# Kernel optimization log

Measured on AMD Instinct MI355X. Metric: run time of the kernel, lower is better.

The kernel has to match this reference:

```python
import jax, jax.numpy as jnp
import numpy as np

N_HEAD = 16
N_KV_HEAD = 4
N_EMBD = 2048
HEAD_DIM = N_EMBD // N_HEAD
RMS_EPS = float(np.finfo(np.float32).eps)  # torch F.rms_norm default eps


def setup_inputs() -> dict:
    key = jax.random.key(0)
    ks = jax.random.split(key, 7)
    B, T = 2, 2048
    s = 0.02
    return {
        "x": jax.random.normal(ks[0], (B, T, N_EMBD), jnp.float32),
        "cos": jax.random.uniform(ks[1], (T, 1, HEAD_DIM), jnp.float32),
        "sin": jax.random.uniform(ks[2], (T, 1, HEAD_DIM), jnp.float32),
        "wq": jax.random.normal(ks[3], (N_HEAD * HEAD_DIM, N_EMBD), jnp.float32) * s,
        "wk": jax.random.normal(ks[4], (N_KV_HEAD * HEAD_DIM, N_EMBD), jnp.float32) * s,
        "wv": jax.random.normal(ks[5], (N_KV_HEAD * HEAD_DIM, N_EMBD), jnp.float32) * s,
        "wproj": jax.random.normal(ks[6], (N_EMBD, N_EMBD), jnp.float32) * s,
    }


def _rotate_half(x):
    h = x.shape[-1] // 2
    return jnp.concatenate([-x[..., h:], x[..., :h]], axis=-1)


def _apply_rope(x, cos, sin):  # x: [B, T, H, D]; cos/sin: [T, 1, D]
    return x * cos + _rotate_half(x) * sin


def _rms_norm(x):
    var = jnp.mean(jnp.square(x), axis=-1, keepdims=True)
    return x * jax.lax.rsqrt(var + RMS_EPS)


def reference(x, cos, sin, wq, wk, wv, wproj):
    B, T, C = x.shape
    group = N_HEAD // N_KV_HEAD
    q = (x @ wq.T).reshape(B, T, N_HEAD, HEAD_DIM)
    k = (x @ wk.T).reshape(B, T, N_KV_HEAD, HEAD_DIM)
    v = (x @ wv.T).reshape(B, T, N_KV_HEAD, HEAD_DIM)
    q = _rms_norm(_apply_rope(q, cos, sin))  # RoPE then QK RMSNorm
    k = _rms_norm(_apply_rope(k, cos, sin))
    # to [B, H, T, D]; expand kv heads for GQA
    q = q.transpose(0, 2, 1, 3)
    k = jnp.repeat(k.transpose(0, 2, 1, 3), group, axis=1)
    v = jnp.repeat(v.transpose(0, 2, 1, 3), group, axis=1)
    scale = 1.0 / jnp.sqrt(jnp.asarray(HEAD_DIM, x.dtype))
    scores = jnp.einsum('bhqd,bhkd->bhqk', q, k) * scale
    causal = jnp.tril(jnp.ones((T, T), bool))
    scores = jnp.where(causal, scores, jnp.asarray(-jnp.inf, scores.dtype))
    attn = jax.nn.softmax(scores, axis=-1)
    y = jnp.einsum('bhqk,bhkd->bhqd', attn, v)
    y = y.transpose(0, 2, 1, 3).reshape(B, T, C)
    return y @ wproj.T
```

## Files before the change

### kernel.cpp

```cpp
#include <hip/hip_runtime.h>
#include <hip/hip_bf16.h>

typedef __hip_bfloat16 bf16;
typedef __attribute__((ext_vector_type(8))) __bf16 bf16x8;
typedef __attribute__((ext_vector_type(4))) float f32x4;

#define MFMA16(a, b, c) __builtin_amdgcn_mfma_f32_16x16x32_bf16((a), (b), (c), 0, 0, 0)

#define BT 4096
#define CE 2048
#define NQKV 3072
#define TSEQ 2048
#define HD 128

#define QSCALE (0.08838834764831845f * 1.4426950408889634f)
#define M2 16.3222f

__device__ __forceinline__ void gld16(const void* g, void* l)
{
    __builtin_amdgcn_global_load_lds(
        (const __attribute__((address_space(1))) void*)g,
        (__attribute__((address_space(3))) void*)l, 16, 0, 0);
}

__global__ void detect_dtype(const unsigned short* __restrict__ x, int* __restrict__ flag)
{
    __shared__ int cnt;
    if (threadIdx.x == 0) cnt = 0;
    __syncthreads();
    unsigned short w = x[2 * threadIdx.x];
    int e = (w >> 7) & 0xFF;
    atomicAdd(&cnt, (e >= 117 && e <= 130) ? 1 : 0);
    __syncthreads();
    if (threadIdx.x == 0) *flag = (cnt < 128) ? 1 : 0;
}

__device__ __forceinline__ void stage8(short* dst, const void* src, size_t eoff, bool f32)
{
    if (f32) {
        const float* s = (const float*)src + eoff;
        float4 f0 = *(const float4*)s;
        float4 f1 = *(const float4*)(s + 4);
        bf16x8 v;
        v[0] = (__bf16)f0.x; v[1] = (__bf16)f0.y; v[2] = (__bf16)f0.z; v[3] = (__bf16)f0.w;
        v[4] = (__bf16)f1.x; v[5] = (__bf16)f1.y; v[6] = (__bf16)f1.z; v[7] = (__bf16)f1.w;
        *(bf16x8*)dst = v;
    } else {
        *(uint4*)dst = *(const uint4*)((const bf16*)src + eoff);
    }
}

__device__ __forceinline__ float ldf(const void* p, int i, bool f32)
{
    return f32 ? ((const float*)p)[i] : __bfloat162float(((const bf16*)p)[i]);
}

__global__ __launch_bounds__(256)
void conv_bf16(const void* __restrict__ src, bf16* __restrict__ dst,
               const int* __restrict__ flagp)
{
    const bool f = *flagp != 0;
    size_t i8 = (size_t)blockIdx.x * 256 + threadIdx.x;
    stage8((short*)(dst + i8 * 8), src, i8 * 8, f);
}

__global__ __launch_bounds__(256)
void gemm_bt(const void* __restrict__ A, const bf16* __restrict__ W,
             void* __restrict__ C, int M, int N, int K, int lda,
             int aGate, int oGate, const int* __restrict__ flagp)
{
    __shared__ short As[128][32];
    __shared__ short Bs[128][32];

    const int f = *flagp;
    const bool aF = aGate && f, oF = oGate && f;

    const int tid   = threadIdx.x;
    const int lane  = tid & 63;
    const int wid   = tid >> 6;
    const int row16 = lane & 15;
    const int quad  = lane >> 4;
    const int wr    = wid >> 1;
    const int wc    = wid & 1;
    const int m0    = blockIdx.y * 128;
    const int n0    = blockIdx.x * 128;

    const int rl4 = wid * 16 + (lane >> 2);
    const int c8  = (lane & 3) * 8;

    f32x4 acc[4][4];
#pragma unroll
    for (int i = 0; i < 4; i++)
#pragma unroll
        for (int j = 0; j < 4; j++)
            acc[i][j] = (f32x4){0.f, 0.f, 0.f, 0.f};

    for (int k0 = 0; k0 < K; k0 += 32) {
#pragma unroll
        for (int i = 0; i < 2; i++) {
            int r = i * 64 + rl4;
            gld16(W + (size_t)(n0 + r) * K + k0 + c8, &Bs[r][c8]);
        }
        if (!aF) {
#pragma unroll
            for (int i = 0; i < 2; i++) {
                int r = i * 64 + rl4;
                gld16((const bf16*)A + (size_t)(m0 + r) * lda + k0 + c8, &As[r][c8]);
            }
        } else {
#pragma unroll
            for (int i = 0; i < 2; i++) {
                int c = i * 256 + tid;
                int row = c >> 2, col = (c & 3) << 3;
                stage8(&As[row][col], A, (size_t)(m0 + row) * lda + k0 + col, true);
            }
        }
        __syncthreads();

        bf16x8 af[4], bfv[4];
#pragma unroll
        for (int mi = 0; mi < 4; mi++)
            af[mi] = *(const bf16x8*)&As[wr * 64 + mi * 16 + row16][quad * 8];
#pragma unroll
        for (int ni = 0; ni < 4; ni++)
            bfv[ni] = *(const bf16x8*)&Bs[wc * 64 + ni * 16 + row16][quad * 8];
#pragma unroll
        for (int mi = 0; mi < 4; mi++)
#pragma unroll
            for (int ni = 0; ni < 4; ni++)
                acc[mi][ni] = MFMA16(af[mi], bfv[ni], acc[mi][ni]);
        __syncthreads();
    }

#pragma unroll
    for (int mi = 0; mi < 4; mi++) {
        int rowb = m0 + wr * 64 + mi * 16 + quad * 4;
#pragma unroll
        for (int ni = 0; ni < 4; ni++) {
            int col = n0 + wc * 64 + ni * 16 + row16;
#pragma unroll
            for (int r = 0; r < 4; r++) {
                size_t idx = (size_t)(rowb + r) * N + col;
                float  v   = acc[mi][ni][r];
                if (oF) ((float*)C)[idx] = v;
                else    ((bf16*)C)[idx]  = __float2bfloat16(v);
            }
        }
    }
}

__global__ __launch_bounds__(256, 2)
void gemm9(const bf16* __restrict__ A, const bf16* __restrict__ W,
           void* __restrict__ C, int M, int N, int K, int lda,
           int oGate, const int* __restrict__ flagp)
{
    __shared__ __bf16 As[3][128][32];
    __shared__ __bf16 Bs[3][256][32];

    const bool oF = oGate && (*flagp != 0);

    const int tid   = threadIdx.x;
    const int lane  = tid & 63;
    const int row16 = lane & 15;
    const int quad  = lane >> 4;
    const int wc    = tid >> 6;
    const int m0    = blockIdx.y * 128;
    const int n0    = blockIdx.x * 256;
    const int NT    = K >> 5;

    const int srow = tid >> 2;
    const int sc   = (tid & 3) ^ (srow & 3);
    const bf16* Ag = A + (size_t)(m0 + srow) * lda + sc * 8;
    const bf16* Bg = W + (size_t)(n0 + srow) * K   + sc * 8;
    char* const AsB = (char*)As;
    char* const BsB = (char*)Bs;
    const int sdst = tid * 16;

    auto stA = [&](int kt, int s) {
#pragma unroll
        for (int u = 0; u < 2; ++u)
            gld16(Ag + (size_t)(u * 64) * lda + kt * 32,
                  AsB + s * 8192 + u * 4096 + sdst);
    };
    auto stB = [&](int kt, int s) {
#pragma unroll
        for (int u = 0; u < 4; ++u)
            gld16(Bg + (size_t)(u * 64) * K + kt * 32,
                  BsB + s * 16384 + u * 4096 + sdst);
    };

    const int swzB  = (quad ^ (row16 & 3)) * 16;
    const int raOff = row16 * 64 + swzB;
    const int rbOff = (wc * 64 + row16) * 64 + swzB;

    f32x4 acc[8][4];
#pragma unroll
    for (int i = 0; i < 8; i++)
#pragma unroll
        for (int j = 0; j < 4; j++)
            acc[i][j] = (f32x4){0.f, 0.f, 0.f, 0.f};

    stA(0, 0); stB(0, 0);
    stA(1, 1); stB(1, 1);
    asm volatile("s_waitcnt vmcnt(6)" ::: "memory");
    __builtin_amdgcn_s_barrier();
    __builtin_amdgcn_sched_barrier(0);

    int sl = 0, sl2 = 2;
    for (int t = 0; t < NT; ++t) {
        const bool pf = (t + 2) < NT;
        const int sbA = sl * 8192, sbB = sl * 16384;

        bf16x8 af0[4], bfr[4];
#pragma unroll
        for (int ni = 0; ni < 4; ni++)
            bfr[ni] = *(const bf16x8*)(BsB + sbB + rbOff + ni * 1024);
#pragma unroll
        for (int mi = 0; mi < 4; mi++)
            af0[mi] = *(const bf16x8*)(AsB + sbA + raOff + mi * 1024);
        if (pf) stB(t + 2, sl2);
        __builtin_amdgcn_s_barrier();
        asm volatile("s_waitcnt lgkmcnt(0)" ::: "memory");
        __builtin_amdgcn_s_setprio(1);
#pragma unroll
        for (int mi = 0; mi < 4; mi++)
#pragma unroll
            for (int ni = 0; ni < 4; ni++)
                acc[mi][ni] = MFMA16(af0[mi], bfr[ni], acc[mi][ni]);
        __builtin_amdgcn_s_setprio(0);
        __builtin_amdgcn_s_barrier();
        __builtin_amdgcn_sched_barrier(0);

        bf16x8 af1[4];
#pragma unroll
        for (int mi = 0; mi < 4; mi++)
            af1[mi] = *(const bf16x8*)(AsB + sbA + raOff + (4 + mi) * 1024);
        if (pf) stA(t + 2, sl2);
        if (t < NT - 2) asm volatile("s_waitcnt vmcnt(6)" ::: "memory");
        else            asm volatile("s_waitcnt vmcnt(0)" ::: "memory");
        __builtin_amdgcn_s_barrier();
        asm volatile("s_waitcnt lgkmcnt(0)" ::: "memory");
        __builtin_amdgcn_s_setprio(1);
#pragma unroll
        for (int mi = 0; mi < 4; mi++)
#pragma unroll
            for (int ni = 0; ni < 4; ni++)
                acc[4 + mi][ni] = MFMA16(af1[mi], bfr[ni], acc[4 + mi][ni]);
        __builtin_amdgcn_s_setprio(0);
        __builtin_amdgcn_s_barrier();
        __builtin_amdgcn_sched_barrier(0);

        sl  = (sl  == 2) ? 0 : sl  + 1;
        sl2 = (sl2 == 2) ? 0 : sl2 + 1;
    }

#pragma unroll
    for (int mi = 0; mi < 8; mi++) {
        int rowb = m0 + mi * 16 + quad * 4;
#pragma unroll
        for (int ni = 0; ni < 4; ni++) {
            int col = n0 + wc * 64 + ni * 16 + row16;
#pragma unroll
            for (int r = 0; r < 4; r++) {
                size_t idx = (size_t)(rowb + r) * N + col;
                float  v   = acc[mi][ni][r];
                if (oF) ((float*)C)[idx] = v;
                else    ((bf16*)C)[idx]  = __float2bfloat16(v);
            }
        }
    }
}

__global__ __launch_bounds__(256)
void rope_rms(bf16* __restrict__ qkv, const void* __restrict__ cosp,
              const void* __restrict__ sinp, const int* __restrict__ flagp)
{
    const bool f = *flagp != 0;
    const int wg   = blockIdx.x * 4 + (threadIdx.x >> 6);
    const int lane = threadIdx.x & 63;
    const int s    = wg % 20;
    const int m    = wg / 20;
    const int t    = m & (TSEQ - 1);

    const int col = (s < 16) ? s * HD : CE + (s - 16) * HD;
    bf16* p = qkv + (size_t)m * NQKV + col;

    float xlo = __bfloat162float(p[lane]);
    float xhi = __bfloat162float(p[lane + 64]);
    float cl  = ldf(cosp, t * HD + lane, f);
    float sl  = ldf(sinp, t * HD + lane, f);
    float ch  = ldf(cosp, t * HD + 64 + lane, f);
    float sh  = ldf(sinp, t * HD + 64 + lane, f);

    float rlo = xlo * cl - xhi * sl;
    float rhi = xhi * ch + xlo * sh;

    float ss = rlo * rlo + rhi * rhi;
#pragma unroll
    for (int off = 32; off > 0; off >>= 1)
        ss += __shfl_xor(ss, off, 64);
    float inv = rsqrtf(ss * (1.0f / 128.0f) + 1.1920929e-07f);
    if (s < 16) inv *= QSCALE;

    p[lane]      = __float2bfloat16(rlo * inv);
    p[lane + 64] = __float2bfloat16(rhi * inv);
}

__global__ __launch_bounds__(256)
void vtrans(const bf16* __restrict__ qkv, bf16* __restrict__ vt)
{
    int idx = blockIdx.x * 256 + threadIdx.x;
    int t  = idx & (TSEQ - 1);
    int d  = (idx >> 11) & 127;
    int bh = idx >> 18;
    vt[idx] = qkv[((size_t)((bh >> 2) * TSEQ + t)) * NQKV + 2560 + (bh & 3) * HD + d];
}

__global__ __launch_bounds__(512, 2)
void attn(bf16* __restrict__ qkv, const bf16* __restrict__ vt)
{
    __shared__ __bf16 Ks[2][64][128];
    __shared__ __bf16 Vs[2][128][64];
    __shared__ __bf16 Pl[8][16][72];

    const int tid   = threadIdx.x;
    const int lane  = tid & 63;
    const int wid   = tid >> 6;
    const int row16 = lane & 15;
    const int quad  = lane >> 4;
    const int b   = blockIdx.y >> 2;
    const int hk  = blockIdx.y & 3;
    const int h   = hk * 4 + (wid & 3);
    const int mh  = wid >> 2;
    const int p   = blockIdx.x;

    const bf16* Kp = qkv + ((size_t)(b * TSEQ)) * NQKV + CE + hk * HD;
    const bf16* Vp = vt + ((size_t)(b * 4 + hk) * HD) * TSEQ;

    char* const KsB = (char*)Ks;
    char* const VsB = (char*)Vs;

    auto stage = [&](int buf, int k0) {
#pragma unroll
        for (int i = 0; i < 2; i++) {
            int kr = (wid << 3) + i * 4 + (lane >> 4);
            int kc = (lane & 15) ^ (kr & 7);
            gld16(Kp + (size_t)(k0 + kr) * NQKV + kc * 8,
                  KsB + buf * 16384 + ((wid << 3) + i * 4) * 256 + lane * 16);
            int vr = (wid << 4) + i * 8 + (lane >> 3);
            int vc = (lane & 7) ^ (vr & 7);
            gld16(Vp + (size_t)vr * TSEQ + k0 + vc * 8,
                  VsB + buf * 16384 + ((wid << 4) + i * 8) * 128 + lane * 16);
        }
    };

    for (int pass = 0; pass < 2; ++pass) {
        const int xi  = pass ? 63 - p : p;
        const int nkt = (xi >> 1) + 1;
        const int qr0 = xi * 32 + mh * 16;

        const bf16* Q = qkv + ((size_t)(b * TSEQ + qr0)) * NQKV + h * HD;
        bf16x8 aq[4];
#pragma unroll
        for (int ds = 0; ds < 4; ds++)
            aq[ds] = *(const bf16x8*)(Q + (size_t)row16 * NQKV + ds * 32 + quad * 8);

        f32x4 o[8];
#pragma unroll
        for (int dt = 0; dt < 8; dt++) o[dt] = (f32x4){0.f, 0.f, 0.f, 0.f};
        float lsum[4] = {0.f, 0.f, 0.f, 0.f};

        __syncthreads();
        stage(0, 0);
        __syncthreads();

        for (int t = 0; t < nkt; ++t) {
            const int cur = t & 1;
            if (t + 1 < nkt) stage(cur ^ 1, (t + 1) * 64);

            f32x4 s[4];
#pragma unroll
            for (int kg = 0; kg < 4; kg++) s[kg] = (f32x4){0.f, 0.f, 0.f, 0.f};
            __builtin_amdgcn_s_setprio(1);
#pragma unroll
            for (int ds = 0; ds < 4; ds++) {
#pragma unroll
                for (int kg = 0; kg < 4; kg++) {
                    int krow = kg * 16 + row16;
                    int phys = (ds * 4 + quad) ^ (row16 & 7);
                    bf16x8 kf = *(const bf16x8*)(KsB + cur * 16384 + krow * 256 + phys * 16);
                    s[kg] = MFMA16(aq[ds], kf, s[kg]);
                }
            }
            __builtin_amdgcn_s_setprio(0);

            const bool diag = (t == nkt - 1);
            const int  k0   = t * 64;
#pragma unroll
            for (int r = 0; r < 4; r++) {
                float pv[4];
                int qrow = qr0 + quad * 4 + r;
#pragma unroll
                for (int kg = 0; kg < 4; kg++) {
                    float e = __builtin_amdgcn_exp2f(s[kg][r] - M2);
                    pv[kg] = (!diag || (k0 + kg * 16 + row16 <= qrow)) ? e : 0.f;
                }
                lsum[r] += (pv[0] + pv[1]) + (pv[2] + pv[3]);
#pragma unroll
                for (int kg = 0; kg < 4; kg++)
                    Pl[wid][quad * 4 + r][kg * 16 + row16] = (__bf16)pv[kg];
            }
            __asm__ volatile("" ::: "memory");

            __builtin_amdgcn_s_setprio(1);
#pragma unroll
            for (int c = 0; c < 2; c++) {
                bf16x8 pf = *(const bf16x8*)&Pl[wid][row16][c * 32 + quad * 8];
#pragma unroll
                for (int dt = 0; dt < 8; dt++) {
                    int vrow = dt * 16 + row16;
                    int phys = (c * 4 + quad) ^ (row16 & 7);
                    bf16x8 vf = *(const bf16x8*)(VsB + cur * 16384 + vrow * 128 + phys * 16);
                    o[dt] = MFMA16(pf, vf, o[dt]);
                }
            }
            __builtin_amdgcn_s_setprio(0);
            __asm__ volatile("" ::: "memory");
            __syncthreads();
        }

#pragma unroll
        for (int r = 0; r < 4; r++) {
            float l = lsum[r];
#pragma unroll
            for (int off = 1; off < 16; off <<= 1)
                l += __shfl_xor(l, off, 64);
            float rl = 1.0f / l;
            int trow = qr0 + quad * 4 + r;
            bf16* dst = qkv + ((size_t)(b * TSEQ + trow)) * NQKV + h * HD;
#pragma unroll
            for (int dt = 0; dt < 8; dt++)
                dst[dt * 16 + row16] = __float2bfloat16(o[dt][r] * rl);
        }
    }
}

extern "C" void kernel_launch(void* const* d_in, const int* in_sizes, int n_in,
                              void* d_out, int out_size, void* d_ws, size_t ws_size,
                              hipStream_t stream)
{
    bf16* qkv   = (bf16*)d_ws;
    bf16* vt    = qkv + (size_t)BT * NQKV;
    bf16* wqkvb = vt + (size_t)2 * 4 * HD * TSEQ;
    int* flagp  = (int*)(wqkvb + (size_t)NQKV * CE);
    bf16* xb    = wqkvb + (size_t)NQKV * CE + 16;

    const size_t need = ((size_t)BT * NQKV + (size_t)2 * 4 * HD * TSEQ
                         + (size_t)NQKV * CE + 16 + (size_t)BT * CE) * sizeof(bf16);
    const bool useXb = ws_size >= need;

    detect_dtype<<<1, 256, 0, stream>>>((const unsigned short*)d_in[0], flagp);

    conv_bf16<<<(2048 * 2048 / 8) / 256, 256, 0, stream>>>(d_in[3], wqkvb, flagp);
    conv_bf16<<<(512 * 2048 / 8) / 256, 256, 0, stream>>>(d_in[4], wqkvb + (size_t)2048 * 2048, flagp);
    conv_bf16<<<(512 * 2048 / 8) / 256, 256, 0, stream>>>(d_in[5], wqkvb + (size_t)2560 * 2048, flagp);

    if (useXb) {
        conv_bf16<<<(BT * CE / 8) / 256, 256, 0, stream>>>(d_in[0], xb, flagp);
        gemm9<<<dim3(NQKV / 256, BT / 128), 256, 0, stream>>>(
            xb, wqkvb, qkv, BT, NQKV, CE, CE, 0, flagp);
    } else {
        gemm_bt<<<dim3(NQKV / 128, BT / 128), 256, 0, stream>>>(
            d_in[0], wqkvb, qkv, BT, NQKV, CE, CE, 1, 0, flagp);
    }

    conv_bf16<<<(2048 * 2048 / 8) / 256, 256, 0, stream>>>(d_in[6], wqkvb, flagp);

    vtrans<<<(2 * 4 * HD * TSEQ) / 256, 256, 0, stream>>>(qkv, vt);

    rope_rms<<<(BT * 20) / 4, 256, 0, stream>>>(qkv, d_in[1], d_in[2], flagp);

    attn<<<dim3(32, 2 * 4), 512, 0, stream>>>(qkv, vt);

    if (useXb) {
        gemm9<<<dim3(CE / 256, BT / 128), 256, 0, stream>>>(
            qkv, wqkvb, d_out, BT, CE, CE, NQKV, 1, flagp);
    } else {
        gemm_bt<<<dim3(CE / 128, BT / 128), 256, 0, stream>>>(
            qkv, wqkvb, d_out, BT, CE, CE, NQKV, 0, 1, flagp);
    }
}
```

Baseline: 340.0 us.

## Replace gemm9 with templated 512-thread GEMM using K=64 tiles and double buffering

Replaces the 256-thread, 3-stage, K=32 GEMM with a templated 512-thread kernel that uses K=64 LDS tiles and double buffering, with a 2x4 wave layout. The QKV projection uses 256-row tiles (MI=8) and the output projection uses 128-row tiles (MI=4). The aim is to raise MFMA work per barrier and cut synchronisation and issue overhead. In exchange, pipeline depth drops to two stages with a full vmcnt(0) wait every iteration, LDS use rises, and the larger QKV tiles mean fewer blocks in flight.

```diff
diff --git a/kernel.cpp b/kernel.cpp
--- a/kernel.cpp
+++ b/kernel.cpp
@@ -149,114 +149,136 @@
     }
 }
 
-__global__ __launch_bounds__(256, 2)
-void gemm9(const bf16* __restrict__ A, const bf16* __restrict__ W,
+template<int MI>
+__global__ __launch_bounds__(512, 2)
+void gemmP(const bf16* __restrict__ A, const bf16* __restrict__ W,
            void* __restrict__ C, int M, int N, int K, int lda,
            int oGate, const int* __restrict__ flagp)
 {
-    __shared__ __bf16 As[3][128][32];
-    __shared__ __bf16 Bs[3][256][32];
+    constexpr int BM     = MI * 32;
+    constexpr int ABYTES = BM * 128;
+    constexpr int AUL    = ABYTES / 8192;
+
+    __shared__ __bf16 As[2][BM][64];
+    __shared__ __bf16 Bs[2][256][64];
 
     const bool oF = oGate && (*flagp != 0);
 
     const int tid   = threadIdx.x;
     const int lane  = tid & 63;
+    const int wid   = tid >> 6;
     const int row16 = lane & 15;
     const int quad  = lane >> 4;
-    const int wc    = tid >> 6;
-    const int m0    = blockIdx.y * 128;
+    const int wr    = wid >> 2;
+    const int wc    = wid & 3;
+    const int m0    = blockIdx.y * BM;
     const int n0    = blockIdx.x * 256;
-    const int NT    = K >> 5;
-
-    const int srow = tid >> 2;
-    const int sc   = (tid & 3) ^ (srow & 3);
-    const bf16* Ag = A + (size_t)(m0 + srow) * lda + sc * 8;
-    const bf16* Bg = W + (size_t)(n0 + srow) * K   + sc * 8;
+    const int NT    = K >> 6;
+
+    const int srow = tid >> 3;
+    const int sc8  = ((tid & 7) ^ (srow & 7)) * 8;
+    const bf16* Ag = A + (size_t)(m0 + srow) * lda + sc8;
+    const bf16* Bg = W + (size_t)(n0 + srow) * K   + sc8;
     char* const AsB = (char*)As;
     char* const BsB = (char*)Bs;
     const int sdst = tid * 16;
 
-    auto stA = [&](int kt, int s) {
-#pragma unroll
-        for (int u = 0; u < 2; ++u)
-            gld16(Ag + (size_t)(u * 64) * lda + kt * 32,
-                  AsB + s * 8192 + u * 4096 + sdst);
+    auto stA = [&](int kt, int b) {
+#pragma unroll
+        for (int u = 0; u < AUL; ++u)
+            gld16(Ag + (size_t)(u * 64) * lda + kt * 64,
+                  AsB + b * ABYTES + u * 8192 + sdst);
     };
-    auto stB = [&](int kt, int s) {
+    auto stB = [&](int kt, int b) {
 #pragma unroll
         for (int u = 0; u < 4; ++u)
-            gld16(Bg + (size_t)(u * 64) * K + kt * 32,
-                  BsB + s * 16384 + u * 4096 + sdst);
+            gld16(Bg + (size_t)(u * 64) * K + kt * 64,
+                  BsB + b * 32768 + u * 8192 + sdst);
     };
 
-    const int swzB  = (quad ^ (row16 & 3)) * 16;
-    const int raOff = row16 * 64 + swzB;
-    const int rbOff = (wc * 64 + row16) * 64 + swzB;
-
-    f32x4 acc[8][4];
-#pragma unroll
-    for (int i = 0; i < 8; i++)
+    const int swz  = ((quad ^ (row16 & 7)) * 16);
+    const int swz1 = (((4 + quad) ^ (row16 & 7)) * 16);
+    const int aRow = wr * (MI * 16) + row16;
+    const int bRow = wc * 64 + row16;
+
+    auto ldA = [&](int b, int mi, int kk) -> bf16x8 {
+        return *(const bf16x8*)(AsB + b * ABYTES + (aRow + mi * 16) * 128
+                                + (kk ? swz1 : swz));
+    };
+    auto ldB = [&](int b, int ni, int kk) -> bf16x8 {
+        return *(const bf16x8*)(BsB + b * 32768 + (bRow + ni * 16) * 128
+                                + (kk ? swz1 : swz));
+    };
+
+    f32x4 acc[MI][4];
+#pragma unroll
+    for (int i = 0; i < MI; i++)
 #pragma unroll
         for (int j = 0; j < 4; j++)
             acc[i][j] = (f32x4){0.f, 0.f, 0.f, 0.f};
 
     stA(0, 0); stB(0, 0);
-    stA(1, 1); stB(1, 1);
-    asm volatile("s_waitcnt vmcnt(6)" ::: "memory");
+    asm volatile("s_waitcnt vmcnt(0)" ::: "memory");
     __builtin_amdgcn_s_barrier();
     __builtin_amdgcn_sched_barrier(0);
 
-    int sl = 0, sl2 = 2;
     for (int t = 0; t < NT; ++t) {
-        const bool pf = (t + 2) < NT;
-        const int sbA = sl * 8192, sbB = sl * 16384;
-
-        bf16x8 af0[4], bfr[4];
+        const int rb = t & 1;
+        const int wb = rb ^ 1;
+
+        bf16x8 bfr[4][2];
 #pragma unroll
         for (int ni = 0; ni < 4; ni++)
-            bfr[ni] = *(const bf16x8*)(BsB + sbB + rbOff + ni * 1024);
-#pragma unroll
-        for (int mi = 0; mi < 4; mi++)
-            af0[mi] = *(const bf16x8*)(AsB + sbA + raOff + mi * 1024);
-        if (pf) stB(t + 2, sl2);
-        __builtin_amdgcn_s_barrier();
-        asm volatile("s_waitcnt lgkmcnt(0)" ::: "memory");
+#pragma unroll
+            for (int kk = 0; kk < 2; kk++)
+                bfr[ni][kk] = ldB(rb, ni, kk);
+        bf16x8 a0[2][2];
+#pragma unroll
+        for (int i = 0; i < 2; i++)
+#pragma unroll
+            for (int kk = 0; kk < 2; kk++)
+                a0[i][kk] = ldA(rb, i, kk);
+
+        if (t + 1 < NT) { stB(t + 1, wb); stA(t + 1, wb); }
+
         __builtin_amdgcn_s_setprio(1);
 #pragma unroll
-        for (int mi = 0; mi < 4; mi++)
-#pragma unroll
-            for (int ni = 0; ni < 4; ni++)
-                acc[mi][ni] = MFMA16(af0[mi], bfr[ni], acc[mi][ni]);
+        for (int kk = 0; kk < 2; kk++)
+#pragma unroll
+            for (int i = 0; i < 2; i++)
+#pragma unroll
+                for (int ni = 0; ni < 4; ni++)
+                    acc[i][ni] = MFMA16(a0[i][kk], bfr[ni][kk], acc[i][ni]);
         __builtin_amdgcn_s_setprio(0);
+
+#pragma unroll
+        for (int p = 1; p < MI / 2; ++p) {
+            bf16x8 ap[2][2];
+#pragma unroll
+            for (int i = 0; i < 2; i++)
+#pragma unroll
+                for (int kk = 0; kk < 2; kk++)
+                    ap[i][kk] = ldA(rb, 2 * p + i, kk);
+            __builtin_amdgcn_s_setprio(1);
+#pragma unroll
+            for (int kk = 0; kk < 2; kk++)
+#pragma unroll
+                for (int i = 0; i < 2; i++)
+#pragma unroll
+                    for (int ni = 0; ni < 4; ni++)
+                        acc[2 * p + i][ni] =
+                            MFMA16(ap[i][kk], bfr[ni][kk], acc[2 * p + i][ni]);
+            __builtin_amdgcn_s_setprio(0);
+        }
+
+        asm volatile("s_waitcnt vmcnt(0)" ::: "memory");
         __builtin_amdgcn_s_barrier();
         __builtin_amdgcn_sched_barrier(0);
-
-        bf16x8 af1[4];
-#pragma unroll
-        for (int mi = 0; mi < 4; mi++)
-            af1[mi] = *(const bf16x8*)(AsB + sbA + raOff + (4 + mi) * 1024);
-        if (pf) stA(t + 2, sl2);
-        if (t < NT - 2) asm volatile("s_waitcnt vmcnt(6)" ::: "memory");
-        else            asm volatile("s_waitcnt vmcnt(0)" ::: "memory");
-        __builtin_amdgcn_s_barrier();
-        asm volatile("s_waitcnt lgkmcnt(0)" ::: "memory");
-        __builtin_amdgcn_s_setprio(1);
-#pragma unroll
-        for (int mi = 0; mi < 4; mi++)
-#pragma unroll
-            for (int ni = 0; ni < 4; ni++)
-                acc[4 + mi][ni] = MFMA16(af1[mi], bfr[ni], acc[4 + mi][ni]);
-        __builtin_amdgcn_s_setprio(0);
-        __builtin_amdgcn_s_barrier();
-        __builtin_amdgcn_sched_barrier(0);
-
-        sl  = (sl  == 2) ? 0 : sl  + 1;
-        sl2 = (sl2 == 2) ? 0 : sl2 + 1;
-    }
-
-#pragma unroll
-    for (int mi = 0; mi < 8; mi++) {
-        int rowb = m0 + mi * 16 + quad * 4;
+    }
+
+#pragma unroll
+    for (int mi = 0; mi < MI; mi++) {
+        int rowb = m0 + wr * (MI * 16) + mi * 16 + quad * 4;
 #pragma unroll
         for (int ni = 0; ni < 4; ni++) {
             int col = n0 + wc * 64 + ni * 16 + row16;
@@ -467,7 +489,7 @@
 
     if (useXb) {
         conv_bf16<<<(BT * CE / 8) / 256, 256, 0, stream>>>(d_in[0], xb, flagp);
-        gemm9<<<dim3(NQKV / 256, BT / 128), 256, 0, stream>>>(
+        gemmP<8><<<dim3(NQKV / 256, BT / 256), 512, 0, stream>>>(
             xb, wqkvb, qkv, BT, NQKV, CE, CE, 0, flagp);
     } else {
         gemm_bt<<<dim3(NQKV / 128, BT / 128), 256, 0, stream>>>(
@@ -483,7 +505,7 @@
     attn<<<dim3(32, 2 * 4), 512, 0, stream>>>(qkv, vt);
 
     if (useXb) {
-        gemm9<<<dim3(CE / 256, BT / 128), 256, 0, stream>>>(
+        gemmP<4><<<dim3(CE / 256, BT / 128), 512, 0, stream>>>(
             qkv, wqkvb, d_out, BT, CE, CE, NQKV, 1, flagp);
     } else {
         gemm_bt<<<dim3(CE / 128, BT / 128), 256, 0, stream>>>(
```

Measured after the change: 330.4 us. 1.03x faster.
